# Performance work log

Hardware: AMD Instinct MI355X
Metric: run time of the kernel (lower is better)

The kernel has to match this reference:

```python
import jax, jax.numpy as jnp
import numpy as np

B, N, M12, H, O, I, DIFF = 8192, 100, 12, 64, 128, 12, 1.0
TWO_PI = 2.0 * np.pi


def _moments_single(xi, K):
    # xi: [N, 2] single sample; K: [12, 2] exponent pairs -> [12]
    xc = xi - xi.mean(axis=0)                 # center per-sample (mean over points)
    p = xc[:, None, :] ** K[None, :, :]       # [N, 12, 2]
    return jnp.sum(p[..., 0] * p[..., 1], axis=0)  # [12]


def setup_inputs() -> dict:
    key = jax.random.key(0)
    ks = jax.random.split(key, 8)
    # 12 integer central-moment exponent pairs (p, q)
    P = jnp.array([1, 2, 0, 2, 1, 3, 0, 2, 3, 1, 4, 0], jnp.float32)
    Q = jnp.array([1, 0, 2, 1, 2, 0, 3, 2, 1, 3, 0, 4], jnp.float32)
    K = jnp.stack([P, Q], axis=-1)            # [12, 2]

    x = jax.random.normal(ks[0], (B, N, 2), jnp.float32)
    t = jax.random.uniform(ks[1], (1,), jnp.float32, 0.1, 1.0)  # positive time
    W_fourier = jax.random.normal(ks[2], (H // 2,), jnp.float32) * 30.0

    def lin(k, fin, fout):
        bound = 1.0 / np.sqrt(fin)
        kw, kb = jax.random.split(k)
        W = jax.random.uniform(kw, (fin, fout), jnp.float32, -bound, bound)
        b = jax.random.uniform(kb, (fout,), jnp.float32, -bound, bound)
        return W, b

    embed_W, embed_b = lin(ks[3], H, H)
    lin1_W, lin1_b = lin(ks[4], I, H)
    lin2a_W, lin2a_b = lin(ks[5], H, O)
    lin2b_W, lin2b_b = lin(ks[6], O, I)
    lin2c_W, lin2c_b = lin(ks[7], I, I)
    return {
        'x': x, 't': t, 'K': K, 'W_fourier': W_fourier,
        'embed_W': embed_W, 'embed_b': embed_b,
        'lin1_W': lin1_W, 'lin1_b': lin1_b,
        'lin2a_W': lin2a_W, 'lin2a_b': lin2a_b,
        'lin2b_W': lin2b_W, 'lin2b_b': lin2b_b,
        'lin2c_W': lin2c_W, 'lin2c_b': lin2c_b,
    }


def reference(x, t, K, W_fourier, embed_W, embed_b, lin1_W, lin1_b,
              lin2a_W, lin2a_b, lin2b_W, lin2b_b, lin2c_W, lin2c_b):
    # Invariance encoding ('Moment' mode): [B, 12]
    m = jax.vmap(_moments_single, in_axes=(0, None))(x, K)
    h = jax.nn.gelu(m @ lin1_W + lin1_b, approximate=False)   # [B, H] (dropout = eval identity)
    # Gaussian Fourier time embedding: [1, H]
    xp = t[:, None] * W_fourier[None, :] * TWO_PI
    emb = jnp.concatenate([jnp.sin(xp), jnp.cos(xp)], axis=-1) @ embed_W + embed_b
    h = jax.nn.gelu((h + emb) @ lin2a_W + lin2a_b, approximate=False)
    h = jax.nn.gelu(h @ lin2b_W + lin2b_b, approximate=False)
    h = (h @ lin2c_W + lin2c_b) / jnp.sqrt(DIFF * t)          # [B, 12]
    # Per-sample jacobian of the moment map: [B, 12, N, 2]
    # (equals the block diagonal of torch.autograd.functional.jacobian over the batch)
    jac = jax.vmap(jax.jacrev(_moments_single), in_axes=(0, None))(x, K)
    # Replaces the (i, j) double loop of tiny matmuls with one batched contraction
    return jnp.einsum('bk,bknj->bnj', h, jac)                 # [B, N, 2]
```

## Files before the change

kernel.cpp:

```cpp
#include <hip/hip_runtime.h>


static __device__ __forceinline__ float gelu_f(float x) {
    float y = 0.7071067811865475f * x;
    float s = fabsf(y);
    float t = __builtin_amdgcn_rcpf(fmaf(0.3275911f, s, 1.0f));
    float p = t * fmaf(t, fmaf(t, fmaf(t, fmaf(t, 1.061405429f,
                    -1.453152027f), 1.421413741f), -0.284496736f), 0.254829592f);
    float e = __expf(-y * y);
    float ea = fmaf(-p, e, 1.0f);
    float erfv = copysignf(ea, y);
    return 0.5f * x * (1.0f + erfv);
}

#define DPP_ADD(v, ctrl) \
    v += __int_as_float(__builtin_amdgcn_update_dpp(0, __float_as_int(v), ctrl, 0xf, 0xf, true))

static __device__ __forceinline__ float wave_sum(float v) {
    DPP_ADD(v, 0x111);
    DPP_ADD(v, 0x112);
    DPP_ADD(v, 0x114);
    DPP_ADD(v, 0x118);
    DPP_ADD(v, 0x142);
    DPP_ADD(v, 0x143);
    return __int_as_float(__builtin_amdgcn_readlane(__float_as_int(v), 63));
}

#define TWO_PI_F 6.283185307179586f

__global__ __launch_bounds__(64) void emb_precompute(
    const float* __restrict__ t_in,
    const float* __restrict__ Wf,
    const float* __restrict__ embW,
    const float* __restrict__ embB,
    float* __restrict__ ws)
{
    __shared__ float s_f[64];
    const int tid = threadIdx.x;
    const float tval = t_in[0];
    if (tid < 32) {
        float xp = tval * Wf[tid] * TWO_PI_F;
        s_f[tid]      = sinf(xp);
        s_f[tid + 32] = cosf(xp);
    }
    __syncthreads();
    float acc = embB[tid];
    const float4* f4 = reinterpret_cast<const float4*>(s_f);
    #pragma unroll
    for (int c = 0; c < 16; ++c) {
        float4 a4 = f4[c];
        int j = 4 * c;
        acc = fmaf(a4.x, embW[(j+0)*64 + tid],
              fmaf(a4.y, embW[(j+1)*64 + tid],
              fmaf(a4.z, embW[(j+2)*64 + tid],
              fmaf(a4.w, embW[(j+3)*64 + tid], acc))));
    }
    ws[tid] = acc;
    if (tid == 0) ws[64] = rsqrtf(tval);
}

__global__ __launch_bounds__(256) void scorenet_fused(
    const float* __restrict__ x,
    const float* __restrict__ emb_ws,
    const float* __restrict__ W1,
    const float* __restrict__ b1,
    const float* __restrict__ W2a,
    const float* __restrict__ b2a,
    const float* __restrict__ W2b,
    const float* __restrict__ b2b,
    const float* __restrict__ W2c,
    const float* __restrict__ b2c,
    float* __restrict__ out,
    int B)
{
    __shared__ float s_a[64][4];
    __shared__ float s_part[4][2][4][64];
    __shared__ float s_w2bT[12][128];

    const int tid = threadIdx.x;
    const int lane = tid & 63;
    const int w = tid >> 6;

    const int b = blockIdx.x * 4 + w;
    const bool valid = b < B;
    const int bc = valid ? b : B - 1;

    const float2* px = reinterpret_cast<const float2*>(x) + (size_t)bc * 100;
    const bool has2 = lane < 36;
    float2 p0 = px[lane];
    float2 p1 = px[has2 ? lane + 64 : lane];

    #pragma unroll
    for (int i = tid; i < 1536; i += 256) {
        int row = i / 12, col = i - row * 12;
        s_w2bT[col][row] = W2b[i];
    }

    const float emb_lane = emb_ws[lane];
    const float rst = emb_ws[64];

    float xa = p0.x, ya = p0.y;
    float xb = has2 ? p1.x : 0.0f;
    float yb = has2 ? p1.y : 0.0f;

    const float mux = wave_sum(xa + xb) * 0.01f;
    const float muy = wave_sum(ya + yb) * 0.01f;

    float ua = xa - mux, va = ya - muy;
    float ub = has2 ? (xb - mux) : 0.0f;
    float vb = has2 ? (yb - muy) : 0.0f;

    float ms[12];
    {
        float u2 = ua * ua, v2 = va * va;
        ms[0] = ua * va;   ms[1] = u2;        ms[2] = v2;
        ms[3] = u2 * va;   ms[4] = ua * v2;
        ms[5] = u2 * ua;   ms[6] = v2 * va;
        ms[7] = u2 * v2;   ms[8] = ms[5] * va; ms[9] = ua * ms[6];
        ms[10] = u2 * u2;  ms[11] = v2 * v2;
        float w2 = ub * ub, z2 = vb * vb;
        ms[0] += ub * vb;  ms[1] += w2;       ms[2] += z2;
        ms[3] += w2 * vb;  ms[4] += ub * z2;
        ms[5] += w2 * ub;  ms[6] += z2 * vb;
        ms[7] += w2 * z2;  ms[8] += w2 * ub * vb; ms[9] += ub * z2 * vb;
        ms[10] += w2 * w2; ms[11] += z2 * z2;
    }
    float m[12];
    #pragma unroll
    for (int k = 0; k < 12; ++k) m[k] = wave_sum(ms[k]);

    float a1 = b1[lane];
    #pragma unroll
    for (int k = 0; k < 12; ++k) a1 = fmaf(m[k], W1[k * 64 + lane], a1);
    float aval = gelu_f(a1) + emb_lane;

    s_a[lane][w] = aval;
    __syncthreads();

    float4 plo = {0.f, 0.f, 0.f, 0.f};
    float4 phi = {0.f, 0.f, 0.f, 0.f};
    {
        const float4* a4p = reinterpret_cast<const float4*>(&s_a[0][0]);
        const float2* w2a2 = reinterpret_cast<const float2*>(W2a);
        #pragma unroll
        for (int jj = 0; jj < 16; ++jj) {
            const int j = (w << 4) + jj;
            float4 a4 = a4p[j];
            float2 ww = w2a2[j * 64 + lane];
            plo.x = fmaf(a4.x, ww.x, plo.x);
            plo.y = fmaf(a4.y, ww.x, plo.y);
            plo.z = fmaf(a4.z, ww.x, plo.z);
            plo.w = fmaf(a4.w, ww.x, plo.w);
            phi.x = fmaf(a4.x, ww.y, phi.x);
            phi.y = fmaf(a4.y, ww.y, phi.y);
            phi.z = fmaf(a4.z, ww.y, phi.z);
            phi.w = fmaf(a4.w, ww.y, phi.w);
        }
    }
    s_part[0][0][w][lane] = plo.x;
    s_part[1][0][w][lane] = plo.y;
    s_part[2][0][w][lane] = plo.z;
    s_part[3][0][w][lane] = plo.w;
    s_part[0][1][w][lane] = phi.x;
    s_part[1][1][w][lane] = phi.y;
    s_part[2][1][w][lane] = phi.z;
    s_part[3][1][w][lane] = phi.w;
    __syncthreads();

    const float2 bb2a = reinterpret_cast<const float2*>(b2a)[lane];
    float acc0 = bb2a.x + ((s_part[w][0][0][lane] + s_part[w][0][1][lane])
                         + (s_part[w][0][2][lane] + s_part[w][0][3][lane]));
    float acc1 = bb2a.y + ((s_part[w][1][0][lane] + s_part[w][1][1][lane])
                         + (s_part[w][1][2][lane] + s_part[w][1][3][lane]));
    float h2lo = gelu_f(acc0), h2hi = gelu_f(acc1);

    float h3[12];
    #pragma unroll
    for (int k = 0; k < 12; ++k) {
        float2 wk = *reinterpret_cast<const float2*>(&s_w2bT[k][2 * lane]);
        float p3 = fmaf(h2lo, wk.x, h2hi * wk.y);
        h3[k] = gelu_f(wave_sum(p3) + b2b[k]);
    }

    float hk = 0.0f;
    if (lane < 12) {
        hk = b2c[lane];
        #pragma unroll
        for (int j = 0; j < 12; ++j) hk = fmaf(h3[j], W2c[j * 12 + lane], hk);
        hk *= rst;
    }
    float h[12];
    #pragma unroll
    for (int k = 0; k < 12; ++k)
        h[k] = __int_as_float(__builtin_amdgcn_readlane(__float_as_int(hk), k));

    const float inv_n = 0.01f;
    float c0 = (2.0f*h[3]*m[0] + h[4]*m[2] + 3.0f*h[5]*m[1] + 2.0f*h[7]*m[4]
              + 3.0f*h[8]*m[3] + h[9]*m[6] + 4.0f*h[10]*m[5]) * inv_n;
    float c1 = (h[3]*m[1] + 2.0f*h[4]*m[0] + 3.0f*h[6]*m[2] + 2.0f*h[7]*m[3]
              + h[8]*m[5] + 3.0f*h[9]*m[4] + 4.0f*h[11]*m[6]) * inv_n;

    const float A1 = 2.0f*h[1], A2 = h[0],      A3 = 3.0f*h[5], A4 = 2.0f*h[3], A5 = h[4];
    const float A6 = 4.0f*h[10],A7 = 3.0f*h[8], A8 = 2.0f*h[7], A9 = h[9];
    const float B1 = h[0],      B2 = 2.0f*h[2], B3 = h[3],      B4 = 2.0f*h[4], B5 = 3.0f*h[6];
    const float B6 = h[8],      B7 = 2.0f*h[7], B8 = 3.0f*h[9], B9 = 4.0f*h[11];

    float2* pout = reinterpret_cast<float2*>(out) + (size_t)bc * 100;
    if (valid) {
        float u = ua, v = va;
        float u2 = u*u, v2 = v*v;
        float o0 = A1*u + A2*v + A3*u2 + A4*u*v + A5*v2 + A6*u2*u + A7*u2*v + A8*u*v2 + A9*v2*v - c0;
        float o1 = B1*u + B2*v + B3*u2 + B4*u*v + B5*v2 + B6*u2*u + B7*u2*v + B8*u*v2 + B9*v2*v - c1;
        float2 r; r.x = o0; r.y = o1;
        pout[lane] = r;
        if (has2) {
            float uu = ub, vv = vb;
            float uu2 = uu*uu, vv2 = vv*vv;
            float q0 = A1*uu + A2*vv + A3*uu2 + A4*uu*vv + A5*vv2 + A6*uu2*uu + A7*uu2*vv + A8*uu*vv2 + A9*vv2*vv - c0;
            float q1 = B1*uu + B2*vv + B3*uu2 + B4*uu*vv + B5*vv2 + B6*uu2*uu + B7*uu2*vv + B8*uu*vv2 + B9*vv2*vv - c1;
            float2 r2; r2.x = q0; r2.y = q1;
            pout[lane + 64] = r2;
        }
    }
}

extern "C" void kernel_launch(void* const* d_in, const int* in_sizes, int n_in,
                              void* d_out, int out_size, void* d_ws, size_t ws_size,
                              hipStream_t stream) {
    const float* x    = (const float*)d_in[0];
    const float* t    = (const float*)d_in[1];
    const float* Wf   = (const float*)d_in[3];
    const float* embW = (const float*)d_in[4];
    const float* embB = (const float*)d_in[5];
    const float* W1   = (const float*)d_in[6];
    const float* b1   = (const float*)d_in[7];
    const float* W2a  = (const float*)d_in[8];
    const float* b2a  = (const float*)d_in[9];
    const float* W2b  = (const float*)d_in[10];
    const float* b2b  = (const float*)d_in[11];
    const float* W2c  = (const float*)d_in[12];
    const float* b2c  = (const float*)d_in[13];

    const int B = in_sizes[0] / 200;
    const int blocks = (B + 3) / 4;
    float* ws = (float*)d_ws;

    emb_precompute<<<1, 64, 0, stream>>>(t, Wf, embW, embB, ws);
    scorenet_fused<<<blocks, 256, 0, stream>>>(
        x, ws, W1, b1, W2a, b2a, W2b, b2b, W2c, b2c,
        (float*)d_out, B);
}
```

Baseline: 99.08 us.

## Fuse time-embedding precompute into main kernel and process two samples per wave

Removes the separate single-block embedding kernel and computes the Fourier time embedding inside every block, with the 64x64 matvec split across the four waves. Each block now handles 8 samples (two per wave, looped), which amortizes the W2b transpose into shared memory and the embedding work over more samples and halves the block count. Both samples' inputs are loaded up front to overlap memory latency. The cost is redundant sin/cos and embedding math in every block, extra barriers, and 1024 blocks instead of 2048, which lowers parallelism.

After: 95.99 us. -3.1%, faster.

```diff
diff --git a/kernel.cpp b/kernel.cpp
--- a/kernel.cpp
+++ b/kernel.cpp
@@ -28,40 +28,12 @@
 
 #define TWO_PI_F 6.283185307179586f
 
-__global__ __launch_bounds__(64) void emb_precompute(
+__global__ __launch_bounds__(256) void scorenet_fused(
+    const float* __restrict__ x,
     const float* __restrict__ t_in,
     const float* __restrict__ Wf,
     const float* __restrict__ embW,
     const float* __restrict__ embB,
-    float* __restrict__ ws)
-{
-    __shared__ float s_f[64];
-    const int tid = threadIdx.x;
-    const float tval = t_in[0];
-    if (tid < 32) {
-        float xp = tval * Wf[tid] * TWO_PI_F;
-        s_f[tid]      = sinf(xp);
-        s_f[tid + 32] = cosf(xp);
-    }
-    __syncthreads();
-    float acc = embB[tid];
-    const float4* f4 = reinterpret_cast<const float4*>(s_f);
-    #pragma unroll
-    for (int c = 0; c < 16; ++c) {
-        float4 a4 = f4[c];
-        int j = 4 * c;
-        acc = fmaf(a4.x, embW[(j+0)*64 + tid],
-              fmaf(a4.y, embW[(j+1)*64 + tid],
-              fmaf(a4.z, embW[(j+2)*64 + tid],
-              fmaf(a4.w, embW[(j+3)*64 + tid], acc))));
-    }
-    ws[tid] = acc;
-    if (tid == 0) ws[64] = rsqrtf(tval);
-}
-
-__global__ __launch_bounds__(256) void scorenet_fused(
-    const float* __restrict__ x,
-    const float* __restrict__ emb_ws,
     const float* __restrict__ W1,
     const float* __restrict__ b1,
     const float* __restrict__ W2a,
@@ -73,6 +45,8 @@
     float* __restrict__ out,
     int B)
 {
+    __shared__ float s_f[64];
+    __shared__ float s_epart[4][64];
     __shared__ float s_a[64][4];
     __shared__ float s_part[4][2][4][64];
     __shared__ float s_w2bT[12][128];
@@ -80,15 +54,20 @@
     const int tid = threadIdx.x;
     const int lane = tid & 63;
     const int w = tid >> 6;
-
-    const int b = blockIdx.x * 4 + w;
-    const bool valid = b < B;
-    const int bc = valid ? b : B - 1;
-
-    const float2* px = reinterpret_cast<const float2*>(x) + (size_t)bc * 100;
+    const float tval = t_in[0];
+
+    const int sb0 = blockIdx.x * 8 + w;
+    const int sb1 = sb0 + 4;
+    const bool v0 = sb0 < B, v1 = sb1 < B;
+    const int c0i = v0 ? sb0 : B - 1;
+    const int c1i = v1 ? sb1 : B - 1;
+
     const bool has2 = lane < 36;
-    float2 p0 = px[lane];
-    float2 p1 = px[has2 ? lane + 64 : lane];
+    const float2* px0 = reinterpret_cast<const float2*>(x) + (size_t)c0i * 100;
+    const float2* px1 = reinterpret_cast<const float2*>(x) + (size_t)c1i * 100;
+    float2 pA[2], pB[2];
+    pA[0] = px0[lane];  pB[0] = px0[has2 ? lane + 64 : lane];
+    pA[1] = px1[lane];  pB[1] = px1[has2 ? lane + 64 : lane];
 
     #pragma unroll
     for (int i = tid; i < 1536; i += 256) {
@@ -96,130 +75,157 @@
         s_w2bT[col][row] = W2b[i];
     }
 
-    const float emb_lane = emb_ws[lane];
-    const float rst = emb_ws[64];
-
-    float xa = p0.x, ya = p0.y;
-    float xb = has2 ? p1.x : 0.0f;
-    float yb = has2 ? p1.y : 0.0f;
-
-    const float mux = wave_sum(xa + xb) * 0.01f;
-    const float muy = wave_sum(ya + yb) * 0.01f;
-
-    float ua = xa - mux, va = ya - muy;
-    float ub = has2 ? (xb - mux) : 0.0f;
-    float vb = has2 ? (yb - muy) : 0.0f;
-
-    float ms[12];
+    if (tid < 32) {
+        float xp = tval * Wf[tid] * TWO_PI_F;
+        s_f[tid]      = sinf(xp);
+        s_f[tid + 32] = cosf(xp);
+    }
+    __syncthreads();
+
     {
-        float u2 = ua * ua, v2 = va * va;
-        ms[0] = ua * va;   ms[1] = u2;        ms[2] = v2;
-        ms[3] = u2 * va;   ms[4] = ua * v2;
-        ms[5] = u2 * ua;   ms[6] = v2 * va;
-        ms[7] = u2 * v2;   ms[8] = ms[5] * va; ms[9] = ua * ms[6];
-        ms[10] = u2 * u2;  ms[11] = v2 * v2;
-        float w2 = ub * ub, z2 = vb * vb;
-        ms[0] += ub * vb;  ms[1] += w2;       ms[2] += z2;
-        ms[3] += w2 * vb;  ms[4] += ub * z2;
-        ms[5] += w2 * ub;  ms[6] += z2 * vb;
-        ms[7] += w2 * z2;  ms[8] += w2 * ub * vb; ms[9] += ub * z2 * vb;
-        ms[10] += w2 * w2; ms[11] += z2 * z2;
-    }
-    float m[12];
+        float ep = 0.0f;
+        #pragma unroll
+        for (int jj = 0; jj < 16; ++jj) {
+            int j = 16 * w + jj;
+            ep = fmaf(s_f[j], embW[j * 64 + lane], ep);
+        }
+        s_epart[w][lane] = ep;
+    }
+    __syncthreads();
+
+    const float embl = embB[lane]
+        + ((s_epart[0][lane] + s_epart[1][lane])
+         + (s_epart[2][lane] + s_epart[3][lane]));
+    const float rst = rsqrtf(tval);
+
+    const float2* w2a2 = reinterpret_cast<const float2*>(W2a);
+    const float2 bb2a = reinterpret_cast<const float2*>(b2a)[lane];
+
     #pragma unroll
-    for (int k = 0; k < 12; ++k) m[k] = wave_sum(ms[k]);
-
-    float a1 = b1[lane];
-    #pragma unroll
-    for (int k = 0; k < 12; ++k) a1 = fmaf(m[k], W1[k * 64 + lane], a1);
-    float aval = gelu_f(a1) + emb_lane;
-
-    s_a[lane][w] = aval;
-    __syncthreads();
-
-    float4 plo = {0.f, 0.f, 0.f, 0.f};
-    float4 phi = {0.f, 0.f, 0.f, 0.f};
-    {
-        const float4* a4p = reinterpret_cast<const float4*>(&s_a[0][0]);
-        const float2* w2a2 = reinterpret_cast<const float2*>(W2a);
-        #pragma unroll
-        for (int jj = 0; jj < 16; ++jj) {
-            const int j = (w << 4) + jj;
-            float4 a4 = a4p[j];
-            float2 ww = w2a2[j * 64 + lane];
-            plo.x = fmaf(a4.x, ww.x, plo.x);
-            plo.y = fmaf(a4.y, ww.x, plo.y);
-            plo.z = fmaf(a4.z, ww.x, plo.z);
-            plo.w = fmaf(a4.w, ww.x, plo.w);
-            phi.x = fmaf(a4.x, ww.y, phi.x);
-            phi.y = fmaf(a4.y, ww.y, phi.y);
-            phi.z = fmaf(a4.z, ww.y, phi.z);
-            phi.w = fmaf(a4.w, ww.y, phi.w);
-        }
-    }
-    s_part[0][0][w][lane] = plo.x;
-    s_part[1][0][w][lane] = plo.y;
-    s_part[2][0][w][lane] = plo.z;
-    s_part[3][0][w][lane] = plo.w;
-    s_part[0][1][w][lane] = phi.x;
-    s_part[1][1][w][lane] = phi.y;
-    s_part[2][1][w][lane] = phi.z;
-    s_part[3][1][w][lane] = phi.w;
-    __syncthreads();
-
-    const float2 bb2a = reinterpret_cast<const float2*>(b2a)[lane];
-    float acc0 = bb2a.x + ((s_part[w][0][0][lane] + s_part[w][0][1][lane])
-                         + (s_part[w][0][2][lane] + s_part[w][0][3][lane]));
-    float acc1 = bb2a.y + ((s_part[w][1][0][lane] + s_part[w][1][1][lane])
-                         + (s_part[w][1][2][lane] + s_part[w][1][3][lane]));
-    float h2lo = gelu_f(acc0), h2hi = gelu_f(acc1);
-
-    float h3[12];
-    #pragma unroll
-    for (int k = 0; k < 12; ++k) {
-        float2 wk = *reinterpret_cast<const float2*>(&s_w2bT[k][2 * lane]);
-        float p3 = fmaf(h2lo, wk.x, h2hi * wk.y);
-        h3[k] = gelu_f(wave_sum(p3) + b2b[k]);
-    }
-
-    float hk = 0.0f;
-    if (lane < 12) {
-        hk = b2c[lane];
-        #pragma unroll
-        for (int j = 0; j < 12; ++j) hk = fmaf(h3[j], W2c[j * 12 + lane], hk);
-        hk *= rst;
-    }
-    float h[12];
-    #pragma unroll
-    for (int k = 0; k < 12; ++k)
-        h[k] = __int_as_float(__builtin_amdgcn_readlane(__float_as_int(hk), k));
-
-    const float inv_n = 0.01f;
-    float c0 = (2.0f*h[3]*m[0] + h[4]*m[2] + 3.0f*h[5]*m[1] + 2.0f*h[7]*m[4]
-              + 3.0f*h[8]*m[3] + h[9]*m[6] + 4.0f*h[10]*m[5]) * inv_n;
-    float c1 = (h[3]*m[1] + 2.0f*h[4]*m[0] + 3.0f*h[6]*m[2] + 2.0f*h[7]*m[3]
-              + h[8]*m[5] + 3.0f*h[9]*m[4] + 4.0f*h[11]*m[6]) * inv_n;
-
-    const float A1 = 2.0f*h[1], A2 = h[0],      A3 = 3.0f*h[5], A4 = 2.0f*h[3], A5 = h[4];
-    const float A6 = 4.0f*h[10],A7 = 3.0f*h[8], A8 = 2.0f*h[7], A9 = h[9];
-    const float B1 = h[0],      B2 = 2.0f*h[2], B3 = h[3],      B4 = 2.0f*h[4], B5 = 3.0f*h[6];
-    const float B6 = h[8],      B7 = 2.0f*h[7], B8 = 3.0f*h[9], B9 = 4.0f*h[11];
-
-    float2* pout = reinterpret_cast<float2*>(out) + (size_t)bc * 100;
-    if (valid) {
-        float u = ua, v = va;
-        float u2 = u*u, v2 = v*v;
-        float o0 = A1*u + A2*v + A3*u2 + A4*u*v + A5*v2 + A6*u2*u + A7*u2*v + A8*u*v2 + A9*v2*v - c0;
-        float o1 = B1*u + B2*v + B3*u2 + B4*u*v + B5*v2 + B6*u2*u + B7*u2*v + B8*u*v2 + B9*v2*v - c1;
-        float2 r; r.x = o0; r.y = o1;
-        pout[lane] = r;
-        if (has2) {
-            float uu = ub, vv = vb;
-            float uu2 = uu*uu, vv2 = vv*vv;
-            float q0 = A1*uu + A2*vv + A3*uu2 + A4*uu*vv + A5*vv2 + A6*uu2*uu + A7*uu2*vv + A8*uu*vv2 + A9*vv2*vv - c0;
-            float q1 = B1*uu + B2*vv + B3*uu2 + B4*uu*vv + B5*vv2 + B6*uu2*uu + B7*uu2*vv + B8*uu*vv2 + B9*vv2*vv - c1;
-            float2 r2; r2.x = q0; r2.y = q1;
-            pout[lane + 64] = r2;
+    for (int g = 0; g < 2; ++g) {
+        const bool valid = g ? v1 : v0;
+        const int bc = g ? c1i : c0i;
+
+        float xa = pA[g].x, ya = pA[g].y;
+        float xb = has2 ? pB[g].x : 0.0f;
+        float yb = has2 ? pB[g].y : 0.0f;
+
+        const float mux = wave_sum(xa + xb) * 0.01f;
+        const float muy = wave_sum(ya + yb) * 0.01f;
+
+        float ua = xa - mux, va = ya - muy;
+        float ub = has2 ? (xb - mux) : 0.0f;
+        float vb = has2 ? (yb - muy) : 0.0f;
+
+        float ms[12];
+        {
+            float u2 = ua * ua, v2 = va * va;
+            ms[0] = ua * va;   ms[1] = u2;        ms[2] = v2;
+            ms[3] = u2 * va;   ms[4] = ua * v2;
+            ms[5] = u2 * ua;   ms[6] = v2 * va;
+            ms[7] = u2 * v2;   ms[8] = ms[5] * va; ms[9] = ua * ms[6];
+            ms[10] = u2 * u2;  ms[11] = v2 * v2;
+            float w2 = ub * ub, z2 = vb * vb;
+            ms[0] += ub * vb;  ms[1] += w2;       ms[2] += z2;
+            ms[3] += w2 * vb;  ms[4] += ub * z2;
+            ms[5] += w2 * ub;  ms[6] += z2 * vb;
+            ms[7] += w2 * z2;  ms[8] += w2 * ub * vb; ms[9] += ub * z2 * vb;
+            ms[10] += w2 * w2; ms[11] += z2 * z2;
+        }
+        float m[12];
+        #pragma unroll
+        for (int k = 0; k < 12; ++k) m[k] = wave_sum(ms[k]);
+
+        float a1 = b1[lane];
+        #pragma unroll
+        for (int k = 0; k < 12; ++k) a1 = fmaf(m[k], W1[k * 64 + lane], a1);
+        float aval = gelu_f(a1) + embl;
+
+        s_a[lane][w] = aval;
+        __syncthreads();
+
+        float4 plo = {0.f, 0.f, 0.f, 0.f};
+        float4 phi = {0.f, 0.f, 0.f, 0.f};
+        {
+            const float4* a4p = reinterpret_cast<const float4*>(&s_a[0][0]);
+            #pragma unroll
+            for (int jj = 0; jj < 16; ++jj) {
+                const int j = (w << 4) + jj;
+                float4 a4 = a4p[j];
+                float2 ww = w2a2[j * 64 + lane];
+                plo.x = fmaf(a4.x, ww.x, plo.x);
+                plo.y = fmaf(a4.y, ww.x, plo.y);
+                plo.z = fmaf(a4.z, ww.x, plo.z);
+                plo.w = fmaf(a4.w, ww.x, plo.w);
+                phi.x = fmaf(a4.x, ww.y, phi.x);
+                phi.y = fmaf(a4.y, ww.y, phi.y);
+                phi.z = fmaf(a4.z, ww.y, phi.z);
+                phi.w = fmaf(a4.w, ww.y, phi.w);
+            }
+        }
+        s_part[0][0][w][lane] = plo.x;
+        s_part[1][0][w][lane] = plo.y;
+        s_part[2][0][w][lane] = plo.z;
+        s_part[3][0][w][lane] = plo.w;
+        s_part[0][1][w][lane] = phi.x;
+        s_part[1][1][w][lane] = phi.y;
+        s_part[2][1][w][lane] = phi.z;
+        s_part[3][1][w][lane] = phi.w;
+        __syncthreads();
+
+        float acc0 = bb2a.x + ((s_part[w][0][0][lane] + s_part[w][0][1][lane])
+                             + (s_part[w][0][2][lane] + s_part[w][0][3][lane]));
+        float acc1 = bb2a.y + ((s_part[w][1][0][lane] + s_part[w][1][1][lane])
+                             + (s_part[w][1][2][lane] + s_part[w][1][3][lane]));
+        float h2lo = gelu_f(acc0), h2hi = gelu_f(acc1);
+
+        float h3[12];
+        #pragma unroll
+        for (int k = 0; k < 12; ++k) {
+            float2 wk = *reinterpret_cast<const float2*>(&s_w2bT[k][2 * lane]);
+            float p3 = fmaf(h2lo, wk.x, h2hi * wk.y);
+            h3[k] = gelu_f(wave_sum(p3) + b2b[k]);
+        }
+
+        float hk = 0.0f;
+        if (lane < 12) {
+            hk = b2c[lane];
+            #pragma unroll
+            for (int j = 0; j < 12; ++j) hk = fmaf(h3[j], W2c[j * 12 + lane], hk);
+            hk *= rst;
+        }
+        float h[12];
+        #pragma unroll
+        for (int k = 0; k < 12; ++k)
+            h[k] = __int_as_float(__builtin_amdgcn_readlane(__float_as_int(hk), k));
+
+        const float inv_n = 0.01f;
+        float cc0 = (2.0f*h[3]*m[0] + h[4]*m[2] + 3.0f*h[5]*m[1] + 2.0f*h[7]*m[4]
+                   + 3.0f*h[8]*m[3] + h[9]*m[6] + 4.0f*h[10]*m[5]) * inv_n;
+        float cc1 = (h[3]*m[1] + 2.0f*h[4]*m[0] + 3.0f*h[6]*m[2] + 2.0f*h[7]*m[3]
+                   + h[8]*m[5] + 3.0f*h[9]*m[4] + 4.0f*h[11]*m[6]) * inv_n;
+
+        const float A1 = 2.0f*h[1], A2 = h[0],      A3 = 3.0f*h[5], A4 = 2.0f*h[3], A5 = h[4];
+        const float A6 = 4.0f*h[10],A7 = 3.0f*h[8], A8 = 2.0f*h[7], A9 = h[9];
+        const float B1 = h[0],      B2 = 2.0f*h[2], B3 = h[3],      B4 = 2.0f*h[4], B5 = 3.0f*h[6];
+        const float B6 = h[8],      B7 = 2.0f*h[7], B8 = 3.0f*h[9], B9 = 4.0f*h[11];
+
+        float2* pout = reinterpret_cast<float2*>(out) + (size_t)bc * 100;
+        if (valid) {
+            float u = ua, v = va;
+            float u2 = u*u, v2 = v*v;
+            float o0 = A1*u + A2*v + A3*u2 + A4*u*v + A5*v2 + A6*u2*u + A7*u2*v + A8*u*v2 + A9*v2*v - cc0;
+            float o1 = B1*u + B2*v + B3*u2 + B4*u*v + B5*v2 + B6*u2*u + B7*u2*v + B8*u*v2 + B9*v2*v - cc1;
+            float2 r; r.x = o0; r.y = o1;
+            pout[lane] = r;
+            if (has2) {
+                float uu = ub, vv = vb;
+                float uu2 = uu*uu, vv2 = vv*vv;
+                float q0 = A1*uu + A2*vv + A3*uu2 + A4*uu*vv + A5*vv2 + A6*uu2*uu + A7*uu2*vv + A8*uu*vv2 + A9*vv2*vv - cc0;
+                float q1 = B1*uu + B2*vv + B3*uu2 + B4*uu*vv + B5*vv2 + B6*uu2*uu + B7*uu2*vv + B8*uu*vv2 + B9*vv2*vv - cc1;
+                float2 r2; r2.x = q0; r2.y = q1;
+                pout[lane + 64] = r2;
+            }
         }
     }
 }
@@ -242,11 +248,9 @@
     const float* b2c  = (const float*)d_in[13];
 
     const int B = in_sizes[0] / 200;
-    const int blocks = (B + 3) / 4;
-    float* ws = (float*)d_ws;
-
-    emb_precompute<<<1, 64, 0, stream>>>(t, Wf, embW, embB, ws);
+    const int blocks = (B + 7) / 8;
+
     scorenet_fused<<<blocks, 256, 0, stream>>>(
-        x, ws, W1, b1, W2a, b2a, W2b, b2b, W2c, b2c,
+        x, t, Wf, embW, embB, W1, b1, W2a, b2a, W2b, b2b, W2c, b2c,
         (float*)d_out, B);
 }
```
